# Kernel optimization log

Hardware: AMD Instinct MI355X
Metric: run time of the kernel (lower is better)

Reference implementation:

```python
import jax, jax.numpy as jnp
import numpy as np

T, B, D_IN, D_H, D_OUT = 128, 256, 256, 1024, 256


def _rand_orth(dim, seed=0):
    rng = np.random.default_rng(seed)
    q, _ = np.linalg.qr(rng.normal(size=(dim, dim)))
    return jnp.asarray(q, dtype=jnp.float32)


def setup_inputs() -> dict:
    key = jax.random.key(0)
    k_xs, k_w1x, k_w2 = jax.random.split(key, 3)
    return {
        "xs": jax.random.normal(k_xs, (T, B, D_IN), dtype=jnp.float32),
        "W1x": 0.1 * jax.random.normal(k_w1x, (D_IN, D_H), dtype=jnp.float32),
        "W1h": _rand_orth(D_H),
        "b1": jnp.zeros((D_H,), dtype=jnp.float32),
        "W2": 0.1 * jax.random.normal(k_w2, (D_H, D_OUT), dtype=jnp.float32),
        "b2": jnp.zeros((), dtype=jnp.float32),
    }


def reference(xs, W1x, W1h, b1, W2, b2):
    # xs: [T, B, D_in]; tanh-RNN recurrence over time, then linear readout.
    h0 = jnp.zeros((xs.shape[1], W1h.shape[0]), dtype=xs.dtype)

    def step(h, x):
        h = jnp.tanh(x @ W1x + h @ W1h + b1)
        return h, None

    h, _ = jax.lax.scan(step, h0, xs)
    return h @ W2 + b2
```

## Files before the change

### kernel.cpp

```cpp
#include <hip/hip_runtime.h>
#include <hip/hip_bf16.h>
#include <math.h>

#define TT   128
#define BB   256
#define DIN  256
#define DH   1024
#define DOUT 256

#define NGM 8
#define MR  32
#define NGN 32
#define NC  32

typedef float  floatx4 __attribute__((ext_vector_type(4)));
typedef short  shortx8 __attribute__((ext_vector_type(8)));
typedef unsigned long long u64;

#define CMASK 0x0001000100010001ULL
#define GSTRIDE 32768

__device__ __forceinline__ short f2bf(float f) {
    union { float f; unsigned u; } v; v.f = f;
    unsigned r = v.u + 0x7fffu + ((v.u >> 16) & 1u);
    return (short)(r >> 16);
}

__device__ __forceinline__ unsigned short bf15e(float v, unsigned bit) {
    union { float f; unsigned u; } x; x.f = v;
    unsigned ua = x.u - (bit << 16);
    unsigned k  = (ua + 0xFFFFu + ((ua >> 17) & 1u)) >> 17;
    return (unsigned short)((k << 1) | bit);
}

__device__ __forceinline__ shortx8 mk8(u64 lo, u64 hi) {
    union { struct { u64 a, b; } s; shortx8 v; } u;
    u.s.a = lo; u.s.b = hi;
    return u.v;
}

__device__ __forceinline__ float fast_tanh(float z) {
    float e = __expf(2.0f * fabsf(z));
    float r = 1.0f - 2.0f / (e + 1.0f);
    return copysignf(r, z);
}

#define AGLD(p)    __hip_atomic_load((p),  __ATOMIC_RELAXED, __HIP_MEMORY_SCOPE_AGENT)
#define AGST(p, v) __hip_atomic_store((p), (v), __ATOMIC_RELAXED, __HIP_MEMORY_SCOPE_AGENT)

#define LD16(buf, base) do { \
    _Pragma("unroll") \
    for (int _j = 0; _j < 8; ++_j) { \
        const u64* _p = (const u64*)(hfr + ((base) + _j) * 512); \
        buf[2 * _j]     = AGLD(_p); \
        buf[2 * _j + 1] = AGLD(_p + 1); \
    } } while (0)
#define OK16(buf, okvar) do { \
    int _o = 1; \
    _Pragma("unroll") \
    for (int _j = 0; _j < 16; ++_j) _o &= ((buf[_j] & CMASK) == pat); \
    okvar = __all(_o); } while (0)
#define WAITVALID(buf, base) do { \
    int _okk; OK16(buf, _okk); \
    while (!_okk) { __builtin_amdgcn_s_sleep(1); LD16(buf, base); OK16(buf, _okk); } \
    } while (0)
#define CONS16(buf, base, accX, accY) do { \
    _Pragma("unroll") \
    for (int _j = 0; _j < 8; ++_j) { \
        shortx8 bfr = mk8(buf[2 * _j], buf[2 * _j + 1]); \
        shortx8 a0 = *(const shortx8*)&WhL[(base) + _j][0][q][lr][0]; \
        shortx8 a1 = *(const shortx8*)&WhL[(base) + _j][1][q][lr][0]; \
        accX = __builtin_amdgcn_mfma_f32_16x16x32_bf16(a0, bfr, accX, 0, 0, 0); \
        accY = __builtin_amdgcn_mfma_f32_16x16x32_bf16(a1, bfr, accY, 0, 0, 0); \
    } } while (0)

__global__ __launch_bounds__(128, 1) void rnn_steps_kernel(
    const float* __restrict__ xs, const float* __restrict__ W1x,
    const float* __restrict__ W1h, const float* __restrict__ b1,
    short* __restrict__ Hbuf)
{
    const int gm  = blockIdx.x;
    const int gn  = blockIdx.y;
    const int tid = threadIdx.x;
    const int w   = tid >> 6;
    const int l   = tid & 63;
    const int lr  = l & 15;
    const int q   = l >> 4;

    const int r0 = gm * MR;
    const int c0 = gn * NC;

    __shared__ short WhL[DH / 32][2][4][16][8];
    for (int idx = tid; idx < (DH / 32) * 2 * 4 * 16; idx += 128) {
        const int c  = idx & 15;
        const int qq = (idx >> 4) & 3;
        const int ct = (idx >> 6) & 1;
        const int ks = idx >> 7;
        shortx8 f;
        #pragma unroll
        for (int j = 0; j < 8; ++j)
            f[j] = f2bf(W1h[(size_t)(ks * 32 + qq * 8 + j) * DH + c0 + ct * 16 + c]);
        *(shortx8*)&WhL[ks][ct][qq][c][0] = f;
    }
    shortx8 wx[2][8];
    #pragma unroll
    for (int ct = 0; ct < 2; ++ct)
        #pragma unroll
        for (int ks = 0; ks < 8; ++ks) {
            shortx8 f;
            #pragma unroll
            for (int j = 0; j < 8; ++j)
                f[j] = f2bf(W1x[(size_t)(ks * 32 + q * 8 + j) * DH + c0 + ct * 16 + lr]);
            wx[ct][ks] = f;
        }
    __syncthreads();

    floatx4 bias[2];
    #pragma unroll
    for (int ct = 0; ct < 2; ++ct)
        #pragma unroll
        for (int r = 0; r < 4; ++r) bias[ct][r] = b1[c0 + ct * 16 + q * 4 + r];

    const int myrow = r0 + w * 16 + lr;
    const size_t HS = (size_t)BB * DH;

    short* const Hg   = Hbuf + gm * GSTRIDE;
    const int rdoff   = w * 16384 + q * 128 + lr * 8;
    const int wroff   = w * 16384 + gn * 512 + (q >> 1) * 128 + lr * 8 + (q & 1) * 4;
    const int proff   = w * 16384 + (l & 31) * 512;

    floatx4 xf[16];
    {
        const float* xrow = xs + (size_t)myrow * DIN + q * 8;
        #pragma unroll
        for (int ks = 0; ks < 8; ++ks) {
            xf[2 * ks]     = *(const floatx4*)(xrow + ks * 32);
            xf[2 * ks + 1] = *(const floatx4*)(xrow + ks * 32 + 4);
        }
    }

    for (int t = 1; t <= TT; ++t) {
        const short* const hfr = Hg + (size_t)((t - 1) & 1) * HS + rdoff;
        const int pc = (t >= 2) ? (1 + ((t - 2) % 15)) : 0;
        const u64 pat = ((u64)(pc & 1)) | ((u64)((pc >> 1) & 1) << 16) |
                        ((u64)((pc >> 2) & 1) << 32) | ((u64)((pc >> 3) & 1) << 48);

        const u64* const pp = (const u64*)(Hg + (size_t)((t - 1) & 1) * HS + proff);
        u64 pv = 0;
        if (t > 1) pv = AGLD(pp);

        floatx4 accA0 = {0.f, 0.f, 0.f, 0.f}, accA1 = {0.f, 0.f, 0.f, 0.f};
        floatx4 accB0 = {0.f, 0.f, 0.f, 0.f}, accB1 = {0.f, 0.f, 0.f, 0.f};

        #pragma unroll
        for (int ks = 0; ks < 8; ++ks) {
            floatx4 x0 = xf[2 * ks], x1 = xf[2 * ks + 1];
            shortx8 b;
            b[0] = f2bf(x0[0]); b[1] = f2bf(x0[1]); b[2] = f2bf(x0[2]); b[3] = f2bf(x0[3]);
            b[4] = f2bf(x1[0]); b[5] = f2bf(x1[1]); b[6] = f2bf(x1[2]); b[7] = f2bf(x1[3]);
            accA0 = __builtin_amdgcn_mfma_f32_16x16x32_bf16(wx[0][ks], b, accA0, 0, 0, 0);
            accA1 = __builtin_amdgcn_mfma_f32_16x16x32_bf16(wx[1][ks], b, accA1, 0, 0, 0);
        }

        if (t < TT) {
            const float* xrow = xs + ((size_t)t * BB + myrow) * DIN + q * 8;
            #pragma unroll
            for (int ks = 0; ks < 8; ++ks) {
                xf[2 * ks]     = *(const floatx4*)(xrow + ks * 32);
                xf[2 * ks + 1] = *(const floatx4*)(xrow + ks * 32 + 4);
            }
        }

        if (t > 1) {
            while (!__all((pv & CMASK) == pat)) {
                __builtin_amdgcn_s_sleep(2);
                pv = AGLD(pp);
            }
            u64 A[16], B[16];
            LD16(A, 0);  LD16(B, 8);
            WAITVALID(A, 0);  CONS16(A, 0,  accA0, accA1);
            LD16(A, 16);
            WAITVALID(B, 8);  CONS16(B, 8,  accB0, accB1);
            LD16(B, 24);
            WAITVALID(A, 16); CONS16(A, 16, accA0, accA1);
            WAITVALID(B, 24); CONS16(B, 24, accB0, accB1);
        }

        {
            const floatx4 acc0 = accA0 + accB0;
            const floatx4 acc1 = accA1 + accB1;
            const int cc = 1 + ((t - 1) % 15);
            short* hp = Hg + (size_t)(t & 1) * HS + wroff;
            u64 p0 = 0, p1 = 0;
            #pragma unroll
            for (int r = 0; r < 4; ++r) {
                const unsigned bit = ((unsigned)cc >> r) & 1u;
                p0 |= ((u64)bf15e(fast_tanh(acc0[r] + bias[0][r]), bit)) << (16 * r);
                p1 |= ((u64)bf15e(fast_tanh(acc1[r] + bias[1][r]), bit)) << (16 * r);
            }
            AGST((u64*)(hp), p0);
            AGST((u64*)(hp + 256), p1);
        }
    }
}

__global__ __launch_bounds__(256) void readout_kernel(
    const short* __restrict__ Hfin, const float* __restrict__ W2,
    const float* __restrict__ b2, float* __restrict__ out)
{
    const int o  = threadIdx.x;
    const int b0 = blockIdx.x * 4;
    __shared__ u64 hs8[4 * DH / 4];
    for (int ch = o; ch < 4 * DH / 4; ch += 256) {
        const int row  = ch >> 8;
        const int col0 = (ch & 255) * 4;
        const int rr   = b0 + row;
        const int gmr  = rr >> 5, rt = (rr >> 4) & 1, lrr = rr & 15;
        const int ks   = col0 >> 5, qq = (col0 >> 3) & 3, j0 = col0 & 7;
        const u64* src = (const u64*)(Hfin + (size_t)gmr * GSTRIDE + rt * 16384 +
                                      ks * 512 + qq * 128 + lrr * 8 + j0);
        hs8[ch] = AGLD(src);
    }
    __syncthreads();
    const unsigned* h0 = (const unsigned*)&hs8[0 * 256];
    const unsigned* h1 = (const unsigned*)&hs8[1 * 256];
    const unsigned* h2 = (const unsigned*)&hs8[2 * 256];
    const unsigned* h3 = (const unsigned*)&hs8[3 * 256];
    float a0 = 0.f, a1 = 0.f, a2 = 0.f, a3 = 0.f;
    for (int k2 = 0; k2 < DH / 2; ++k2) {
        float w0 = W2[(2 * k2)     * DOUT + o];
        float w1 = W2[(2 * k2 + 1) * DOUT + o];
        unsigned p0 = h0[k2], p1 = h1[k2], p2 = h2[k2], p3 = h3[k2];
        a0 += __builtin_bit_cast(float, p0 << 16) * w0 + __builtin_bit_cast(float, p0 & 0xffff0000u) * w1;
        a1 += __builtin_bit_cast(float, p1 << 16) * w0 + __builtin_bit_cast(float, p1 & 0xffff0000u) * w1;
        a2 += __builtin_bit_cast(float, p2 << 16) * w0 + __builtin_bit_cast(float, p2 & 0xffff0000u) * w1;
        a3 += __builtin_bit_cast(float, p3 << 16) * w0 + __builtin_bit_cast(float, p3 & 0xffff0000u) * w1;
    }
    const float bias = b2[0];
    out[(b0 + 0) * DOUT + o] = a0 + bias;
    out[(b0 + 1) * DOUT + o] = a1 + bias;
    out[(b0 + 2) * DOUT + o] = a2 + bias;
    out[(b0 + 3) * DOUT + o] = a3 + bias;
}

extern "C" void kernel_launch(void* const* d_in, const int* in_sizes, int n_in,
                              void* d_out, int out_size, void* d_ws, size_t ws_size,
                              hipStream_t stream) {
    (void)in_sizes; (void)n_in; (void)out_size; (void)ws_size;
    const float* xs  = (const float*)d_in[0];
    const float* W1x = (const float*)d_in[1];
    const float* W1h = (const float*)d_in[2];
    const float* b1  = (const float*)d_in[3];
    const float* W2  = (const float*)d_in[4];
    const float* b2  = (const float*)d_in[5];
    float* out = (float*)d_out;

    short* Hbuf = (short*)d_ws;

    rnn_steps_kernel<<<dim3(NGM, NGN), 128, 0, stream>>>(xs, W1x, W1h, b1, Hbuf);
    readout_kernel<<<dim3(BB / 4), 256, 0, stream>>>(Hbuf, W2, b2, out);
}
```

Before: 674.4 us.

## Widen per-block hidden-column tile to 64, halving recurrent grid blocks

Each block now computes 64 hidden columns instead of 32, so the grid shrinks from 256 to 128 persistent blocks. The recurrent W1h slice moves to 128 KB of dynamic LDS, and each consumed h fragment feeds four MFMAs instead of two. The aim is to cut the number of blocks polling and reloading the shared hidden state each step, reducing global-memory traffic and synchronisation fan-in. In exchange, each block does twice the serial MFMA work per step, and register pressure rises with wx[4][8] and eight accumulators.

```diff
diff --git a/kernel.cpp b/kernel.cpp
--- a/kernel.cpp
+++ b/kernel.cpp
@@ -10,8 +10,8 @@
 
 #define NGM 8
 #define MR  32
-#define NGN 32
-#define NC  32
+#define NGN 16
+#define NC  64
 
 typedef float  floatx4 __attribute__((ext_vector_type(4)));
 typedef short  shortx8 __attribute__((ext_vector_type(8)));
@@ -19,6 +19,8 @@
 
 #define CMASK 0x0001000100010001ULL
 #define GSTRIDE 32768
+
+#define WHL(ks, ct, qq, c) ((((ks) * 16 + (ct) * 4 + (qq)) * 128) + (c) * 8)
 
 __device__ __forceinline__ short f2bf(float f) {
     union { float f; unsigned u; } v; v.f = f;
@@ -64,14 +66,18 @@
     int _okk; OK16(buf, _okk); \
     while (!_okk) { __builtin_amdgcn_s_sleep(1); LD16(buf, base); OK16(buf, _okk); } \
     } while (0)
-#define CONS16(buf, base, accX, accY) do { \
+#define CONS16(buf, base, acc) do { \
     _Pragma("unroll") \
     for (int _j = 0; _j < 8; ++_j) { \
         shortx8 bfr = mk8(buf[2 * _j], buf[2 * _j + 1]); \
-        shortx8 a0 = *(const shortx8*)&WhL[(base) + _j][0][q][lr][0]; \
-        shortx8 a1 = *(const shortx8*)&WhL[(base) + _j][1][q][lr][0]; \
-        accX = __builtin_amdgcn_mfma_f32_16x16x32_bf16(a0, bfr, accX, 0, 0, 0); \
-        accY = __builtin_amdgcn_mfma_f32_16x16x32_bf16(a1, bfr, accY, 0, 0, 0); \
+        shortx8 a0 = *(const shortx8*)&WhL[WHL((base) + _j, 0, q, lr)]; \
+        shortx8 a1 = *(const shortx8*)&WhL[WHL((base) + _j, 1, q, lr)]; \
+        shortx8 a2 = *(const shortx8*)&WhL[WHL((base) + _j, 2, q, lr)]; \
+        shortx8 a3 = *(const shortx8*)&WhL[WHL((base) + _j, 3, q, lr)]; \
+        acc[0] = __builtin_amdgcn_mfma_f32_16x16x32_bf16(a0, bfr, acc[0], 0, 0, 0); \
+        acc[1] = __builtin_amdgcn_mfma_f32_16x16x32_bf16(a1, bfr, acc[1], 0, 0, 0); \
+        acc[2] = __builtin_amdgcn_mfma_f32_16x16x32_bf16(a2, bfr, acc[2], 0, 0, 0); \
+        acc[3] = __builtin_amdgcn_mfma_f32_16x16x32_bf16(a3, bfr, acc[3], 0, 0, 0); \
     } } while (0)
 
 __global__ __launch_bounds__(128, 1) void rnn_steps_kernel(
@@ -90,21 +96,21 @@
     const int r0 = gm * MR;
     const int c0 = gn * NC;
 
-    __shared__ short WhL[DH / 32][2][4][16][8];
-    for (int idx = tid; idx < (DH / 32) * 2 * 4 * 16; idx += 128) {
+    extern __shared__ __align__(16) short WhL[];
+    for (int idx = tid; idx < (DH / 32) * 4 * 4 * 16; idx += 128) {
         const int c  = idx & 15;
         const int qq = (idx >> 4) & 3;
-        const int ct = (idx >> 6) & 1;
-        const int ks = idx >> 7;
+        const int ct = (idx >> 6) & 3;
+        const int ks = idx >> 8;
         shortx8 f;
         #pragma unroll
         for (int j = 0; j < 8; ++j)
             f[j] = f2bf(W1h[(size_t)(ks * 32 + qq * 8 + j) * DH + c0 + ct * 16 + c]);
-        *(shortx8*)&WhL[ks][ct][qq][c][0] = f;
-    }
-    shortx8 wx[2][8];
+        *(shortx8*)&WhL[WHL(ks, ct, qq, c)] = f;
+    }
+    shortx8 wx[4][8];
     #pragma unroll
-    for (int ct = 0; ct < 2; ++ct)
+    for (int ct = 0; ct < 4; ++ct)
         #pragma unroll
         for (int ks = 0; ks < 8; ++ks) {
             shortx8 f;
@@ -115,9 +121,9 @@
         }
     __syncthreads();
 
-    floatx4 bias[2];
+    floatx4 bias[4];
     #pragma unroll
-    for (int ct = 0; ct < 2; ++ct)
+    for (int ct = 0; ct < 4; ++ct)
         #pragma unroll
         for (int r = 0; r < 4; ++r) bias[ct][r] = b1[c0 + ct * 16 + q * 4 + r];
 
@@ -126,7 +132,7 @@
 
     short* const Hg   = Hbuf + gm * GSTRIDE;
     const int rdoff   = w * 16384 + q * 128 + lr * 8;
-    const int wroff   = w * 16384 + gn * 512 + (q >> 1) * 128 + lr * 8 + (q & 1) * 4;
+    const int wrbase  = w * 16384 + (q >> 1) * 128 + lr * 8 + (q & 1) * 4;
     const int proff   = w * 16384 + (l & 31) * 512;
 
     floatx4 xf[16];
@@ -149,8 +155,12 @@
         u64 pv = 0;
         if (t > 1) pv = AGLD(pp);
 
-        floatx4 accA0 = {0.f, 0.f, 0.f, 0.f}, accA1 = {0.f, 0.f, 0.f, 0.f};
-        floatx4 accB0 = {0.f, 0.f, 0.f, 0.f}, accB1 = {0.f, 0.f, 0.f, 0.f};
+        floatx4 accA[4], accB[4];
+        #pragma unroll
+        for (int ct = 0; ct < 4; ++ct) {
+            accA[ct] = (floatx4){0.f, 0.f, 0.f, 0.f};
+            accB[ct] = (floatx4){0.f, 0.f, 0.f, 0.f};
+        }
 
         #pragma unroll
         for (int ks = 0; ks < 8; ++ks) {
@@ -158,8 +168,10 @@
             shortx8 b;
             b[0] = f2bf(x0[0]); b[1] = f2bf(x0[1]); b[2] = f2bf(x0[2]); b[3] = f2bf(x0[3]);
             b[4] = f2bf(x1[0]); b[5] = f2bf(x1[1]); b[6] = f2bf(x1[2]); b[7] = f2bf(x1[3]);
-            accA0 = __builtin_amdgcn_mfma_f32_16x16x32_bf16(wx[0][ks], b, accA0, 0, 0, 0);
-            accA1 = __builtin_amdgcn_mfma_f32_16x16x32_bf16(wx[1][ks], b, accA1, 0, 0, 0);
+            accA[0] = __builtin_amdgcn_mfma_f32_16x16x32_bf16(wx[0][ks], b, accA[0], 0, 0, 0);
+            accA[1] = __builtin_amdgcn_mfma_f32_16x16x32_bf16(wx[1][ks], b, accA[1], 0, 0, 0);
+            accA[2] = __builtin_amdgcn_mfma_f32_16x16x32_bf16(wx[2][ks], b, accA[2], 0, 0, 0);
+            accA[3] = __builtin_amdgcn_mfma_f32_16x16x32_bf16(wx[3][ks], b, accA[3], 0, 0, 0);
         }
 
         if (t < TT) {
@@ -178,28 +190,28 @@
             }
             u64 A[16], B[16];
             LD16(A, 0);  LD16(B, 8);
-            WAITVALID(A, 0);  CONS16(A, 0,  accA0, accA1);
+            WAITVALID(A, 0);  CONS16(A, 0,  accA);
             LD16(A, 16);
-            WAITVALID(B, 8);  CONS16(B, 8,  accB0, accB1);
+            WAITVALID(B, 8);  CONS16(B, 8,  accB);
             LD16(B, 24);
-            WAITVALID(A, 16); CONS16(A, 16, accA0, accA1);
-            WAITVALID(B, 24); CONS16(B, 24, accB0, accB1);
+            WAITVALID(A, 16); CONS16(A, 16, accA);
+            WAITVALID(B, 24); CONS16(B, 24, accB);
         }
 
         {
-            const floatx4 acc0 = accA0 + accB0;
-            const floatx4 acc1 = accA1 + accB1;
             const int cc = 1 + ((t - 1) % 15);
-            short* hp = Hg + (size_t)(t & 1) * HS + wroff;
-            u64 p0 = 0, p1 = 0;
+            short* const hp_base = Hg + (size_t)(t & 1) * HS + wrbase;
             #pragma unroll
-            for (int r = 0; r < 4; ++r) {
-                const unsigned bit = ((unsigned)cc >> r) & 1u;
-                p0 |= ((u64)bf15e(fast_tanh(acc0[r] + bias[0][r]), bit)) << (16 * r);
-                p1 |= ((u64)bf15e(fast_tanh(acc1[r] + bias[1][r]), bit)) << (16 * r);
+            for (int ct = 0; ct < 4; ++ct) {
+                const floatx4 acc = accA[ct] + accB[ct];
+                u64 p = 0;
+                #pragma unroll
+                for (int r = 0; r < 4; ++r) {
+                    const unsigned bit = ((unsigned)cc >> r) & 1u;
+                    p |= ((u64)bf15e(fast_tanh(acc[r] + bias[ct][r]), bit)) << (16 * r);
+                }
+                AGST((u64*)(hp_base + (gn * 2 + (ct >> 1)) * 512 + (ct & 1) * 256), p);
             }
-            AGST((u64*)(hp), p0);
-            AGST((u64*)(hp + 256), p1);
         }
     }
 }
@@ -257,6 +269,13 @@
 
     short* Hbuf = (short*)d_ws;
 
-    rnn_steps_kernel<<<dim3(NGM, NGN), 128, 0, stream>>>(xs, W1x, W1h, b1, Hbuf);
+    static bool lds_attr_done = false;
+    if (!lds_attr_done) {
+        hipFuncSetAttribute(reinterpret_cast<const void*>(rnn_steps_kernel),
+                            hipFuncAttributeMaxDynamicSharedMemorySize, 131072);
+        lds_attr_done = true;
+    }
+
+    rnn_steps_kernel<<<dim3(NGM, NGN), 128, 131072, stream>>>(xs, W1x, W1h, b1, Hbuf);
     readout_kernel<<<dim3(BB / 4), 256, 0, stream>>>(Hbuf, W2, b2, out);
 }
```

Result: slower. 906.3 us (+34.4%).
